# Kernel optimization log

Measured on AMD Instinct MI355X. Metric: run time of the kernel, lower is better.

Reference implementation:

```python
import jax, jax.numpy as jnp
import numpy as np

TOP_K = 2


def setup_inputs() -> dict:
    key = jax.random.key(0)
    k1, k2, k3, k4 = jax.random.split(key, 4)
    B, D, H, E = 16384, 1024, 1024, 8
    return {
        "x": jax.random.normal(k1, (B, D), dtype=jnp.float32),
        "Wv": jax.random.normal(k2, (E, D, H), dtype=jnp.float32),
        "Wg": jax.random.normal(k3, (E, D, H), dtype=jnp.float32),
        "gate_w": jax.random.normal(k4, (E, D), dtype=jnp.float32) * (1.0 / np.sqrt(D)),
        "gate_b": jnp.zeros((E,), dtype=jnp.float32),
    }


def reference(x, Wv, Wg, gate_w, gate_b):
    # Router: softmax over expert logits, then top-k selection.
    logits = x @ gate_w.T + gate_b                      # [B, E]
    probs = jax.nn.softmax(logits, axis=1)
    topk_scores, topk_idx = jax.lax.top_k(probs, TOP_K)  # [B, K]

    B, E = probs.shape
    # Scatter top-k scores into a dense [B, E] combine matrix (zeros elsewhere).
    combine = jnp.zeros((B, E), dtype=probs.dtype).at[
        jnp.arange(B)[:, None], topk_idx
    ].add(topk_scores)

    # Dense per-expert SwiGLU; combine matrix zeros out non-selected experts,
    # so the math matches the grouped-gemm top-k dispatch exactly.
    v = jnp.einsum("bd,edh->beh", x, Wv)                # [B, E, H]
    g = jnp.einsum("bd,edh->beh", x, Wg)                # [B, E, H]
    act = v * jax.nn.sigmoid(g)                         # SwiGLU-style gating
    return jnp.einsum("be,beh->bh", combine, act)       # weighted combine [B, H]
```

## Files before the change

### kernel.cpp

```cpp
#include <hip/hip_runtime.h>

#define D_DIM 1024
#define H_DIM 1024
#define E_NUM 8
#define BM 128
#define BN 128
#define BK 64
#define CAP 5120
#define RT_TOK 32

typedef __attribute__((ext_vector_type(8))) _Float16 h8v;
typedef __attribute__((ext_vector_type(4))) float f4v;

__device__ __forceinline__ unsigned short f2h(float f) {
  union { _Float16 h; unsigned short u; } c;
  c.h = (_Float16)f;
  return c.u;
}

__device__ __forceinline__ void gl2lds16(const void* g, void* l) {
  __builtin_amdgcn_global_load_lds(
      (const __attribute__((address_space(1))) unsigned int*)g,
      (__attribute__((address_space(3))) unsigned int*)l, 16, 0, 0);
}

__global__ __launch_bounds__(256) void transpose_w_kernel(
    const float* __restrict__ Wv, const float* __restrict__ Wg,
    unsigned short* __restrict__ Wvt, unsigned short* __restrict__ Wgt) {
  __shared__ float tile[64][65];
  int z = blockIdx.z;
  const float* W = (z & 1) ? Wg : Wv;
  unsigned short* Wt = (z & 1) ? Wgt : Wvt;
  int e = z >> 1;
  int h0 = blockIdx.x * 64, d0 = blockIdx.y * 64;
  const float* Wp = W + (size_t)e * D_DIM * H_DIM;
  unsigned short* Wtp = Wt + (size_t)e * H_DIM * D_DIM;
  int t = threadIdx.x;
#pragma unroll
  for (int j = 0; j < 4; j++) {
    int id = t + 256 * j;
    int dd = id >> 4, hc = id & 15;
    float4 v = *(const float4*)(Wp + (size_t)(d0 + dd) * H_DIM + h0 + hc * 4);
    tile[dd][hc * 4 + 0] = v.x;
    tile[dd][hc * 4 + 1] = v.y;
    tile[dd][hc * 4 + 2] = v.z;
    tile[dd][hc * 4 + 3] = v.w;
  }
  __syncthreads();
#pragma unroll
  for (int j = 0; j < 2; j++) {
    int id = t + 256 * j;
    int h_ = id >> 3, dc = id & 7;
    unsigned short tmp[8];
#pragma unroll
    for (int k = 0; k < 8; k++) tmp[k] = f2h(tile[dc * 8 + k][h_]);
    *(uint4*)(Wtp + (size_t)(h0 + h_) * D_DIM + d0 + dc * 8) = *(uint4*)tmp;
  }
}

__global__ __launch_bounds__(256) void router_kernel(
    const float4* __restrict__ x4, const float4* __restrict__ gw4,
    const float* __restrict__ gb, int* __restrict__ counts,
    int* __restrict__ bucket, float* __restrict__ scoreB,
    int* __restrict__ slotOf, ushort4* __restrict__ xh4, int B) {
  __shared__ float4 gwS[E_NUM * 256];
  __shared__ short eSelS[RT_TOK][2];
  __shared__ float sSelS[RT_TOK][2];
  __shared__ int lCnt[E_NUM], lBase[E_NUM];
  __shared__ unsigned char lOff[RT_TOK][2];
  int tid = threadIdx.x;
  for (int i = tid; i < E_NUM * 256; i += 256) gwS[i] = gw4[i];
  if (tid < E_NUM) lCnt[tid] = 0;
  __syncthreads();
  int wid = tid >> 6, lane = tid & 63;
  for (int rep = 0; rep < RT_TOK / 4; rep++) {
    int t = wid * (RT_TOK / 4) + rep;
    int b = blockIdx.x * RT_TOK + t;
    float acc[E_NUM];
#pragma unroll
    for (int e = 0; e < E_NUM; e++) acc[e] = 0.0f;
#pragma unroll
    for (int i = 0; i < 4; i++) {
      float4 xv = x4[(size_t)b * 256 + i * 64 + lane];
      ushort4 o;
      o.x = f2h(xv.x); o.y = f2h(xv.y); o.z = f2h(xv.z); o.w = f2h(xv.w);
      xh4[(size_t)b * 256 + i * 64 + lane] = o;
#pragma unroll
      for (int e = 0; e < E_NUM; e++) {
        float4 w = gwS[e * 256 + i * 64 + lane];
        acc[e] += xv.x * w.x + xv.y * w.y + xv.z * w.z + xv.w * w.w;
      }
    }
#pragma unroll
    for (int e = 0; e < E_NUM; e++) {
#pragma unroll
      for (int off = 32; off > 0; off >>= 1) acc[e] += __shfl_down(acc[e], off);
    }
    if (lane == 0) {
      float l[E_NUM];
#pragma unroll
      for (int e = 0; e < E_NUM; e++) l[e] = acc[e] + gb[e];
      int i0 = 0;
#pragma unroll
      for (int e = 1; e < E_NUM; e++) if (l[e] > l[i0]) i0 = e;
      int i1 = (i0 == 0) ? 1 : 0;
#pragma unroll
      for (int e = 0; e < E_NUM; e++) if (e != i0 && l[e] > l[i1]) i1 = e;
      float mx = l[i0];
      float denom = 0.0f;
#pragma unroll
      for (int e = 0; e < E_NUM; e++) denom += __expf(l[e] - mx);
      eSelS[t][0] = (short)i0; sSelS[t][0] = 1.0f / denom;
      eSelS[t][1] = (short)i1; sSelS[t][1] = __expf(l[i1] - mx) / denom;
    }
  }
  __syncthreads();
  if (tid < RT_TOK) {
    lOff[tid][0] = (unsigned char)atomicAdd(&lCnt[eSelS[tid][0]], 1);
    lOff[tid][1] = (unsigned char)atomicAdd(&lCnt[eSelS[tid][1]], 1);
  }
  __syncthreads();
  if (tid < E_NUM) lBase[tid] = atomicAdd(&counts[tid * 32], lCnt[tid]);
  __syncthreads();
  if (tid < RT_TOK) {
    int b = blockIdx.x * RT_TOK + tid;
#pragma unroll
    for (int j = 0; j < 2; j++) {
      int e = eSelS[tid][j];
      int pos = lBase[e] + lOff[tid][j];
      if (pos < CAP) {
        int slot = e * CAP + pos;
        bucket[slot] = b;
        scoreB[slot] = sSelS[tid][j];
        slotOf[b * 2 + j] = slot;
      }
    }
  }
}

template <bool USE_PARTIAL>
__global__ __launch_bounds__(256, 2) void moe_gemm_kernel(
    const unsigned short* __restrict__ xh, const unsigned short* __restrict__ Wvt,
    const unsigned short* __restrict__ Wgt, const int* __restrict__ counts,
    const int* __restrict__ bucket, const float* __restrict__ scoreB,
    _Float16* __restrict__ partial, float* __restrict__ out, int B) {
  int e = blockIdx.z;
  int cnt = counts[e * 32];
  int m0 = blockIdx.x * BM;
  if (m0 >= cnt) return;
  int n0 = blockIdx.y * BN;

  __shared__ unsigned short As[BM * BK];
  __shared__ unsigned short Bvs[BN * BK];
  __shared__ unsigned short Bgs[BN * BK];
  __shared__ int tokS[BM];
  __shared__ float scS[BM];

  int tid = threadIdx.x;
  if (tid < BM) {
    int gr = m0 + tid;
    bool vld = gr < cnt;
    tokS[tid] = vld ? bucket[e * CAP + gr] : 0;
    scS[tid] = vld ? scoreB[e * CAP + gr] : 0.0f;
  }
  __syncthreads();

  int wid = tid >> 6, lane = tid & 63;
  int wm = wid & 1, wn = wid >> 1;
  int quad = lane >> 4, lr = lane & 15;

  const unsigned short* Bv0 = Wvt + (size_t)(e * H_DIM + n0) * D_DIM;
  const unsigned short* Bg0 = Wgt + (size_t)(e * H_DIM + n0) * D_DIM;

  int cswh = ((lane & 7) ^ (lane >> 3)) * 8;
  const unsigned short *pA[4], *pBv[4], *pBg[4];
  char *lD[4];
#pragma unroll
  for (int i = 0; i < 4; i++) {
    int W = wid * 4 + i;
    int row = W * 8 + (lane >> 3);
    pA[i] = xh + (size_t)tokS[row] * D_DIM + cswh;
    pBv[i] = Bv0 + (size_t)row * D_DIM + cswh;
    pBg[i] = Bg0 + (size_t)row * D_DIM + cswh;
    lD[i] = (char*)nullptr + W * 1024;
  }

  f4v accv[4][4], accg[4][4];
#pragma unroll
  for (int a = 0; a < 4; a++)
#pragma unroll
    for (int bb = 0; bb < 4; bb++) {
      f4v z = {0.f, 0.f, 0.f, 0.f};
      accv[a][bb] = z;
      accg[a][bb] = z;
    }

  for (int kt = 0; kt < D_DIM / BK; kt++) {
#pragma unroll
    for (int i = 0; i < 4; i++) {
      size_t w = (size_t)(lD[i] - (char*)nullptr);
      gl2lds16(pA[i], (char*)As + w);
      gl2lds16(pBv[i], (char*)Bvs + w);
      gl2lds16(pBg[i], (char*)Bgs + w);
      pA[i] += BK; pBv[i] += BK; pBg[i] += BK;
    }
    __syncthreads();

    h8v af[4][2], bfr[4][2];
#pragma unroll
    for (int fm = 0; fm < 4; fm++)
#pragma unroll
      for (int s = 0; s < 2; s++) {
        int row = wm * 64 + fm * 16 + lr;
        int c = s * 4 + quad;
        af[fm][s] = *(const h8v*)(As + row * BK + ((c ^ (row & 7)) * 8));
      }
#pragma unroll
    for (int fn = 0; fn < 4; fn++)
#pragma unroll
      for (int s = 0; s < 2; s++) {
        int row = wn * 64 + fn * 16 + lr;
        int c = s * 4 + quad;
        bfr[fn][s] = *(const h8v*)(Bvs + row * BK + ((c ^ (row & 7)) * 8));
      }
#pragma unroll
    for (int fm = 0; fm < 4; fm++)
#pragma unroll
      for (int fn = 0; fn < 4; fn++)
#pragma unroll
        for (int s = 0; s < 2; s++)
          accv[fm][fn] = __builtin_amdgcn_mfma_f32_16x16x32_f16(
              af[fm][s], bfr[fn][s], accv[fm][fn], 0, 0, 0);
#pragma unroll
    for (int fn = 0; fn < 4; fn++)
#pragma unroll
      for (int s = 0; s < 2; s++) {
        int row = wn * 64 + fn * 16 + lr;
        int c = s * 4 + quad;
        bfr[fn][s] = *(const h8v*)(Bgs + row * BK + ((c ^ (row & 7)) * 8));
      }
#pragma unroll
    for (int fm = 0; fm < 4; fm++)
#pragma unroll
      for (int fn = 0; fn < 4; fn++)
#pragma unroll
        for (int s = 0; s < 2; s++)
          accg[fm][fn] = __builtin_amdgcn_mfma_f32_16x16x32_f16(
              af[fm][s], bfr[fn][s], accg[fm][fn], 0, 0, 0);
    __syncthreads();
  }

#pragma unroll
  for (int fm = 0; fm < 4; fm++) {
#pragma unroll
    for (int r = 0; r < 4; r++) {
      int row = wm * 64 + fm * 16 + quad * 4 + r;
      float sc = scS[row];
      if (USE_PARTIAL) {
        int slot = e * CAP + m0 + row;
        _Float16* pr = partial + (size_t)slot * H_DIM;
#pragma unroll
        for (int fn = 0; fn < 4; fn++) {
          int col = n0 + wn * 64 + fn * 16 + lr;
          float v = accv[fm][fn][r];
          float g = accg[fm][fn][r];
          pr[col] = (_Float16)(v * sc / (1.0f + __expf(-g)));
        }
      } else {
        int tok = tokS[row];
#pragma unroll
        for (int fn = 0; fn < 4; fn++) {
          int col = n0 + wn * 64 + fn * 16 + lr;
          float v = accv[fm][fn][r];
          float g = accg[fm][fn][r];
          atomicAdd(&out[(size_t)tok * H_DIM + col], v * sc / (1.0f + __expf(-g)));
        }
      }
    }
  }
}

__global__ __launch_bounds__(256) void gather_kernel(
    const _Float16* __restrict__ partial, const int* __restrict__ slotOf,
    float* __restrict__ out) {
  int b = blockIdx.x * 2 + (threadIdx.x >> 7);
  int t = threadIdx.x & 127;
  int s0 = slotOf[b * 2], s1 = slotOf[b * 2 + 1];
  if ((unsigned)s0 >= E_NUM * CAP) s0 = 0;
  if ((unsigned)s1 >= E_NUM * CAP) s1 = 0;
  h8v a = ((const h8v*)(partial + (size_t)s0 * H_DIM))[t];
  h8v c = ((const h8v*)(partial + (size_t)s1 * H_DIM))[t];
  float4 o0, o1;
  o0.x = (float)a[0] + (float)c[0];
  o0.y = (float)a[1] + (float)c[1];
  o0.z = (float)a[2] + (float)c[2];
  o0.w = (float)a[3] + (float)c[3];
  o1.x = (float)a[4] + (float)c[4];
  o1.y = (float)a[5] + (float)c[5];
  o1.z = (float)a[6] + (float)c[6];
  o1.w = (float)a[7] + (float)c[7];
  float4* op = (float4*)(out + (size_t)b * H_DIM);
  op[t * 2] = o0;
  op[t * 2 + 1] = o1;
}

extern "C" void kernel_launch(void* const* d_in, const int* in_sizes, int n_in,
                              void* d_out, int out_size, void* d_ws, size_t ws_size,
                              hipStream_t stream) {
  const float* x = (const float*)d_in[0];
  const float* Wv = (const float*)d_in[1];
  const float* Wg = (const float*)d_in[2];
  const float* gw = (const float*)d_in[3];
  const float* gb = (const float*)d_in[4];
  float* out = (float*)d_out;
  const int B = in_sizes[0] / D_DIM;

  char* ws = (char*)d_ws;
  unsigned short* xh = (unsigned short*)ws;
  size_t off = (size_t)B * D_DIM * 2;
  unsigned short* Wvt = (unsigned short*)(ws + off);
  off += (size_t)E_NUM * H_DIM * D_DIM * 2;
  unsigned short* Wgt = (unsigned short*)(ws + off);
  off += (size_t)E_NUM * H_DIM * D_DIM * 2;
  int* counts = (int*)(ws + off);
  off += 4096;
  int* bucket = (int*)(ws + off);
  off += (size_t)E_NUM * CAP * 4;
  float* scoreB = (float*)(ws + off);
  off += (size_t)E_NUM * CAP * 4;
  int* slotOf = (int*)(ws + off);
  off += (size_t)B * 2 * 4;
  _Float16* partial = (_Float16*)(ws + off);
  size_t need = off + (size_t)E_NUM * CAP * H_DIM * 2;
  bool use_partial = ws_size >= need;

  hipMemsetAsync(counts, 0, 4096, stream);
  if (!use_partial) hipMemsetAsync(d_out, 0, (size_t)out_size * 4, stream);

  router_kernel<<<B / RT_TOK, 256, 0, stream>>>(
      (const float4*)x, (const float4*)gw, gb, counts, bucket, scoreB, slotOf,
      (ushort4*)xh, B);
  transpose_w_kernel<<<dim3(H_DIM / 64, D_DIM / 64, 2 * E_NUM), 256, 0, stream>>>(
      Wv, Wg, Wvt, Wgt);
  if (use_partial) {
    moe_gemm_kernel<true><<<dim3(CAP / BM, H_DIM / BN, E_NUM), 256, 0, stream>>>(
        xh, Wvt, Wgt, counts, bucket, scoreB, partial, out, B);
    gather_kernel<<<B / 2, 256, 0, stream>>>(partial, slotOf, out);
  } else {
    moe_gemm_kernel<false><<<dim3(CAP / BM, H_DIM / BN, E_NUM), 256, 0, stream>>>(
        xh, Wvt, Wgt, counts, bucket, scoreB, partial, out, B);
  }
}
```

Before: 347.8 us.

## Interleave Wv/Wg weights and double-buffer 256x256 GEMM tiles with 8 waves

The transpose kernel now writes Wv and Wg into one combined weight matrix, interleaved in 16-column groups, so the GEMM treats v and g as a single N=2048 problem. The GEMM moves to 256x256 tiles with 512 threads and double-buffered LDS. Global-to-LDS loads for the next K tile are issued in quarters between MFMA phases, using barriers, vmcnt waits and setprio to overlap loads with compute. The goal is less LDS traffic per FLOP and hidden memory latency, at the cost of more registers and LDS per block, fewer blocks and more padded work when expert counts are not multiples of 256.

```diff
diff --git a/kernel.cpp b/kernel.cpp
--- a/kernel.cpp
+++ b/kernel.cpp
@@ -3,9 +3,10 @@
 #define D_DIM 1024
 #define H_DIM 1024
 #define E_NUM 8
-#define BM 128
-#define BN 128
+#define BM 256
+#define BN 256
 #define BK 64
+#define NT (D_DIM / BK)
 #define CAP 5120
 #define RT_TOK 32
 
@@ -26,15 +27,15 @@
 
 __global__ __launch_bounds__(256) void transpose_w_kernel(
     const float* __restrict__ Wv, const float* __restrict__ Wg,
-    unsigned short* __restrict__ Wvt, unsigned short* __restrict__ Wgt) {
+    unsigned short* __restrict__ Wc) {
   __shared__ float tile[64][65];
   int z = blockIdx.z;
   const float* W = (z & 1) ? Wg : Wv;
-  unsigned short* Wt = (z & 1) ? Wgt : Wvt;
+  int mat = z & 1;
   int e = z >> 1;
   int h0 = blockIdx.x * 64, d0 = blockIdx.y * 64;
   const float* Wp = W + (size_t)e * D_DIM * H_DIM;
-  unsigned short* Wtp = Wt + (size_t)e * H_DIM * D_DIM;
+  unsigned short* Wcp = Wc + (size_t)e * (2 * H_DIM) * D_DIM;
   int t = threadIdx.x;
 #pragma unroll
   for (int j = 0; j < 4; j++) {
@@ -54,7 +55,9 @@
     unsigned short tmp[8];
 #pragma unroll
     for (int k = 0; k < 8; k++) tmp[k] = f2h(tile[dc * 8 + k][h_]);
-    *(uint4*)(Wtp + (size_t)(h0 + h_) * D_DIM + d0 + dc * 8) = *(uint4*)tmp;
+    int hg = h0 + h_;
+    int ng = ((hg >> 4) << 5) | (mat << 4) | (hg & 15);
+    *(uint4*)(Wcp + (size_t)ng * D_DIM + d0 + dc * 8) = *(uint4*)tmp;
   }
 }
 
@@ -138,21 +141,52 @@
   }
 }
 
+#define READ_AF(RBASE)                                                         \
+  {                                                                            \
+    _Pragma("unroll") for (int m = 0; m < 4; m++) {                            \
+      _Pragma("unroll") for (int s = 0; s < 2; s++) {                          \
+        int row = (RBASE) + m * 16 + lr;                                       \
+        int c = s * 4 + quad;                                                  \
+        af[m][s] = *(const h8v*)(Ac + row * BK + ((c ^ (row & 7)) << 3));      \
+      }                                                                        \
+    }                                                                          \
+  }
+#define READ_BF(RBASE)                                                         \
+  {                                                                            \
+    _Pragma("unroll") for (int n = 0; n < 2; n++) {                            \
+      _Pragma("unroll") for (int s = 0; s < 2; s++) {                          \
+        int row = (RBASE) + n * 16 + lr;                                       \
+        int c = s * 4 + quad;                                                  \
+        bf[n][s] = *(const h8v*)(Bc + row * BK + ((c ^ (row & 7)) << 3));      \
+      }                                                                        \
+    }                                                                          \
+  }
+#define MFMA_Q(MO, NO)                                                         \
+  {                                                                            \
+    _Pragma("unroll") for (int m = 0; m < 4; m++) {                            \
+      _Pragma("unroll") for (int n = 0; n < 2; n++) {                          \
+        _Pragma("unroll") for (int s = 0; s < 2; s++) {                        \
+          acc[(MO) + m][(NO) + n] = __builtin_amdgcn_mfma_f32_16x16x32_f16(    \
+              af[m][s], bf[n][s], acc[(MO) + m][(NO) + n], 0, 0, 0);           \
+        }                                                                      \
+      }                                                                        \
+    }                                                                          \
+  }
+
 template <bool USE_PARTIAL>
-__global__ __launch_bounds__(256, 2) void moe_gemm_kernel(
-    const unsigned short* __restrict__ xh, const unsigned short* __restrict__ Wvt,
-    const unsigned short* __restrict__ Wgt, const int* __restrict__ counts,
-    const int* __restrict__ bucket, const float* __restrict__ scoreB,
-    _Float16* __restrict__ partial, float* __restrict__ out, int B) {
+__global__ __launch_bounds__(512, 2) void moe_gemm_kernel(
+    const unsigned short* __restrict__ xh, const unsigned short* __restrict__ Wc,
+    const int* __restrict__ counts, const int* __restrict__ bucket,
+    const float* __restrict__ scoreB, _Float16* __restrict__ partial,
+    float* __restrict__ out, int B) {
   int e = blockIdx.z;
   int cnt = counts[e * 32];
   int m0 = blockIdx.x * BM;
   if (m0 >= cnt) return;
   int n0 = blockIdx.y * BN;
 
-  __shared__ unsigned short As[BM * BK];
-  __shared__ unsigned short Bvs[BN * BK];
-  __shared__ unsigned short Bgs[BN * BK];
+  __shared__ unsigned short As[2][BM * BK];
+  __shared__ unsigned short Bs[2][BN * BK];
   __shared__ int tokS[BM];
   __shared__ float scS[BM];
 
@@ -169,111 +203,118 @@
   int wm = wid & 1, wn = wid >> 1;
   int quad = lane >> 4, lr = lane & 15;
 
-  const unsigned short* Bv0 = Wvt + (size_t)(e * H_DIM + n0) * D_DIM;
-  const unsigned short* Bg0 = Wgt + (size_t)(e * H_DIM + n0) * D_DIM;
-
-  int cswh = ((lane & 7) ^ (lane >> 3)) * 8;
-  const unsigned short *pA[4], *pBv[4], *pBg[4];
-  char *lD[4];
+  int rA = tid >> 3;
+  int ksw = ((tid & 7) ^ (rA & 7)) * 8;
+  const unsigned short* WcE = Wc + (size_t)e * (2 * H_DIM) * D_DIM;
+  const unsigned short* pA[4];
+  const unsigned short* pB[4];
 #pragma unroll
   for (int i = 0; i < 4; i++) {
-    int W = wid * 4 + i;
-    int row = W * 8 + (lane >> 3);
-    pA[i] = xh + (size_t)tokS[row] * D_DIM + cswh;
-    pBv[i] = Bv0 + (size_t)row * D_DIM + cswh;
-    pBg[i] = Bg0 + (size_t)row * D_DIM + cswh;
-    lD[i] = (char*)nullptr + W * 1024;
-  }
-
-  f4v accv[4][4], accg[4][4];
-#pragma unroll
-  for (int a = 0; a < 4; a++)
-#pragma unroll
-    for (int bb = 0; bb < 4; bb++) {
-      f4v z = {0.f, 0.f, 0.f, 0.f};
-      accv[a][bb] = z;
-      accg[a][bb] = z;
-    }
-
-  for (int kt = 0; kt < D_DIM / BK; kt++) {
-#pragma unroll
-    for (int i = 0; i < 4; i++) {
-      size_t w = (size_t)(lD[i] - (char*)nullptr);
-      gl2lds16(pA[i], (char*)As + w);
-      gl2lds16(pBv[i], (char*)Bvs + w);
-      gl2lds16(pBg[i], (char*)Bgs + w);
-      pA[i] += BK; pBv[i] += BK; pBg[i] += BK;
-    }
-    __syncthreads();
-
-    h8v af[4][2], bfr[4][2];
-#pragma unroll
-    for (int fm = 0; fm < 4; fm++)
-#pragma unroll
-      for (int s = 0; s < 2; s++) {
-        int row = wm * 64 + fm * 16 + lr;
-        int c = s * 4 + quad;
-        af[fm][s] = *(const h8v*)(As + row * BK + ((c ^ (row & 7)) * 8));
-      }
-#pragma unroll
-    for (int fn = 0; fn < 4; fn++)
-#pragma unroll
-      for (int s = 0; s < 2; s++) {
-        int row = wn * 64 + fn * 16 + lr;
-        int c = s * 4 + quad;
-        bfr[fn][s] = *(const h8v*)(Bvs + row * BK + ((c ^ (row & 7)) * 8));
-      }
-#pragma unroll
-    for (int fm = 0; fm < 4; fm++)
-#pragma unroll
-      for (int fn = 0; fn < 4; fn++)
-#pragma unroll
-        for (int s = 0; s < 2; s++)
-          accv[fm][fn] = __builtin_amdgcn_mfma_f32_16x16x32_f16(
-              af[fm][s], bfr[fn][s], accv[fm][fn], 0, 0, 0);
-#pragma unroll
-    for (int fn = 0; fn < 4; fn++)
-#pragma unroll
-      for (int s = 0; s < 2; s++) {
-        int row = wn * 64 + fn * 16 + lr;
-        int c = s * 4 + quad;
-        bfr[fn][s] = *(const h8v*)(Bgs + row * BK + ((c ^ (row & 7)) * 8));
-      }
-#pragma unroll
-    for (int fm = 0; fm < 4; fm++)
-#pragma unroll
-      for (int fn = 0; fn < 4; fn++)
-#pragma unroll
-        for (int s = 0; s < 2; s++)
-          accg[fm][fn] = __builtin_amdgcn_mfma_f32_16x16x32_f16(
-              af[fm][s], bfr[fn][s], accg[fm][fn], 0, 0, 0);
-    __syncthreads();
-  }
-
-#pragma unroll
-  for (int fm = 0; fm < 4; fm++) {
+    pA[i] = xh + (size_t)tokS[i * 64 + rA] * D_DIM + ksw;
+    pB[i] = WcE + (size_t)(n0 + i * 64 + rA) * D_DIM + ksw;
+  }
+  int dst0 = tid * 8;
+
+  f4v acc[8][4];
+#pragma unroll
+  for (int m = 0; m < 8; m++)
+#pragma unroll
+    for (int n = 0; n < 4; n++) acc[m][n] = (f4v){0.f, 0.f, 0.f, 0.f};
+
+  gl2lds16(pA[0], &As[0][0 * 4096 + dst0]);
+  gl2lds16(pA[1], &As[0][1 * 4096 + dst0]);
+  gl2lds16(pB[0], &Bs[0][0 * 4096 + dst0]);
+  gl2lds16(pB[1], &Bs[0][1 * 4096 + dst0]);
+  gl2lds16(pA[2], &As[0][2 * 4096 + dst0]);
+  gl2lds16(pA[3], &As[0][3 * 4096 + dst0]);
+  gl2lds16(pB[2], &Bs[0][2 * 4096 + dst0]);
+  gl2lds16(pB[3], &Bs[0][3 * 4096 + dst0]);
+#pragma unroll
+  for (int i = 0; i < 4; i++) { pA[i] += BK; pB[i] += BK; }
+  asm volatile("s_waitcnt vmcnt(4)" ::: "memory");
+  __builtin_amdgcn_s_barrier();
+
+  h8v af[4][2], bf[2][2];
+  int cb = 0;
+  for (int kt = 0; kt < NT; ++kt) {
+    int nb = cb ^ 1;
+    const unsigned short* Ac = As[cb];
+    const unsigned short* Bc = Bs[cb];
+    unsigned short* An = As[nb];
+    unsigned short* Bn = Bs[nb];
+
+    READ_AF(wm * 64);
+    READ_BF(wn * 32);
+    gl2lds16(pA[0], An + 0 * 4096 + dst0);
+    gl2lds16(pA[1], An + 1 * 4096 + dst0);
+    __builtin_amdgcn_s_barrier();
+    __builtin_amdgcn_s_setprio(1);
+    MFMA_Q(0, 0);
+    __builtin_amdgcn_s_setprio(0);
+    asm volatile("s_waitcnt vmcnt(4)" ::: "memory");
+    __builtin_amdgcn_s_barrier();
+
+    READ_AF(128 + wm * 64);
+    gl2lds16(pB[0], Bn + 0 * 4096 + dst0);
+    gl2lds16(pB[1], Bn + 1 * 4096 + dst0);
+    __builtin_amdgcn_s_barrier();
+    __builtin_amdgcn_s_setprio(1);
+    MFMA_Q(4, 0);
+    __builtin_amdgcn_s_setprio(0);
+    asm volatile("s_waitcnt vmcnt(4)" ::: "memory");
+    __builtin_amdgcn_s_barrier();
+
+    READ_BF(128 + wn * 32);
+    gl2lds16(pA[2], An + 2 * 4096 + dst0);
+    gl2lds16(pA[3], An + 3 * 4096 + dst0);
+    __builtin_amdgcn_s_barrier();
+    __builtin_amdgcn_s_setprio(1);
+    MFMA_Q(4, 2);
+    __builtin_amdgcn_s_setprio(0);
+    __builtin_amdgcn_s_barrier();
+
+    READ_AF(wm * 64);
+    gl2lds16(pB[2], Bn + 2 * 4096 + dst0);
+    gl2lds16(pB[3], Bn + 3 * 4096 + dst0);
+    __builtin_amdgcn_s_barrier();
+    __builtin_amdgcn_s_setprio(1);
+    MFMA_Q(0, 2);
+    __builtin_amdgcn_s_setprio(0);
+    asm volatile("s_waitcnt vmcnt(4)" ::: "memory");
+    __builtin_amdgcn_s_barrier();
+
+    cb = nb;
+    if (kt < NT - 2) {
+#pragma unroll
+      for (int i = 0; i < 4; i++) { pA[i] += BK; pB[i] += BK; }
+    }
+  }
+  asm volatile("s_waitcnt vmcnt(0)" ::: "memory");
+
+  int hb = blockIdx.y * 128 + wn * 16 + lr;
+#pragma unroll
+  for (int m = 0; m < 8; m++) {
+    int rb = ((m < 4) ? (wm * 64 + m * 16) : (128 + wm * 64 + (m - 4) * 16)) + quad * 4;
 #pragma unroll
     for (int r = 0; r < 4; r++) {
-      int row = wm * 64 + fm * 16 + quad * 4 + r;
-      float sc = scS[row];
+      int rr = rb + r;
+      float sc = scS[rr];
       if (USE_PARTIAL) {
-        int slot = e * CAP + m0 + row;
-        _Float16* pr = partial + (size_t)slot * H_DIM;
-#pragma unroll
-        for (int fn = 0; fn < 4; fn++) {
-          int col = n0 + wn * 64 + fn * 16 + lr;
-          float v = accv[fm][fn][r];
-          float g = accg[fm][fn][r];
-          pr[col] = (_Float16)(v * sc / (1.0f + __expf(-g)));
+        _Float16* pr = partial + (size_t)(e * CAP + m0 + rr) * H_DIM;
+#pragma unroll
+        for (int p = 0; p < 2; p++) {
+          float v = acc[m][2 * p][r];
+          float g = acc[m][2 * p + 1][r];
+          pr[hb + p * 64] = (_Float16)(v * sc / (1.0f + __expf(-g)));
         }
       } else {
-        int tok = tokS[row];
-#pragma unroll
-        for (int fn = 0; fn < 4; fn++) {
-          int col = n0 + wn * 64 + fn * 16 + lr;
-          float v = accv[fm][fn][r];
-          float g = accg[fm][fn][r];
-          atomicAdd(&out[(size_t)tok * H_DIM + col], v * sc / (1.0f + __expf(-g)));
+        int tok = tokS[rr];
+#pragma unroll
+        for (int p = 0; p < 2; p++) {
+          float v = acc[m][2 * p][r];
+          float g = acc[m][2 * p + 1][r];
+          atomicAdd(&out[(size_t)tok * H_DIM + hb + p * 64],
+                    v * sc / (1.0f + __expf(-g)));
         }
       }
     }
@@ -318,10 +359,8 @@
   char* ws = (char*)d_ws;
   unsigned short* xh = (unsigned short*)ws;
   size_t off = (size_t)B * D_DIM * 2;
-  unsigned short* Wvt = (unsigned short*)(ws + off);
-  off += (size_t)E_NUM * H_DIM * D_DIM * 2;
-  unsigned short* Wgt = (unsigned short*)(ws + off);
-  off += (size_t)E_NUM * H_DIM * D_DIM * 2;
+  unsigned short* Wc = (unsigned short*)(ws + off);
+  off += (size_t)E_NUM * (2 * H_DIM) * D_DIM * 2;
   int* counts = (int*)(ws + off);
   off += 4096;
   int* bucket = (int*)(ws + off);
@@ -341,13 +380,13 @@
       (const float4*)x, (const float4*)gw, gb, counts, bucket, scoreB, slotOf,
       (ushort4*)xh, B);
   transpose_w_kernel<<<dim3(H_DIM / 64, D_DIM / 64, 2 * E_NUM), 256, 0, stream>>>(
-      Wv, Wg, Wvt, Wgt);
+      Wv, Wg, Wc);
   if (use_partial) {
-    moe_gemm_kernel<true><<<dim3(CAP / BM, H_DIM / BN, E_NUM), 256, 0, stream>>>(
-        xh, Wvt, Wgt, counts, bucket, scoreB, partial, out, B);
+    moe_gemm_kernel<true><<<dim3(CAP / BM, (2 * H_DIM) / BN, E_NUM), 512, 0, stream>>>(
+        xh, Wc, counts, bucket, scoreB, partial, out, B);
     gather_kernel<<<B / 2, 256, 0, stream>>>(partial, slotOf, out);
   } else {
-    moe_gemm_kernel<false><<<dim3(CAP / BM, H_DIM / BN, E_NUM), 256, 0, stream>>>(
-        xh, Wvt, Wgt, counts, bucket, scoreB, partial, out, B);
-  }
-}
+    moe_gemm_kernel<false><<<dim3(CAP / BM, (2 * H_DIM) / BN, E_NUM), 512, 0, stream>>>(
+        xh, Wc, counts, bucket, scoreB, partial, out, B);
+  }
+}
```

Measured after the change: 372.3 us. +7.0%, slower.
